# Kernel optimization log

Hardware: AMD Instinct MI355X
Metric: run time of the kernel (lower is better)

The kernel has to match this reference:

```python
import jax, jax.numpy as jnp
import numpy as np

N = 4096          # batch of anchors
D = 128           # embedding dim
M = 4             # instances per class (balanced batch) -> 3 positives per anchor
MARGIN = 1.0
INF = jnp.float32(1e30)


def setup_inputs() -> dict:
    key = jax.random.key(0)
    inputs = jax.random.normal(key, (N, D), dtype=jnp.float32)
    targets = (jnp.arange(N, dtype=jnp.int32) // M).astype(jnp.int32)
    return {"inputs": inputs, "targets": targets}


def _forward(inputs, targets, key):
    n = inputs.shape[0]
    k_pos = M - 1            # positives per anchor (and multinomial draw count)
    k_neg = n - M            # negatives per anchor

    # euclidean_dist: ||xi||^2 + ||xj||^2 - 2 xi.xj, clamped and sqrt'ed
    sq = jnp.sum(inputs * inputs, axis=1)
    dist = sq[:, None] + sq[None, :] - 2.0 * (inputs @ inputs.T)
    dist = jnp.sqrt(jnp.clip(dist, 1e-12, None))

    same = targets[:, None] == targets[None, :]
    eye = jnp.eye(n, dtype=bool)
    pos_mask = same & ~eye
    neg_mask = ~same

    # balanced batch -> exactly k_pos positives / k_neg negatives per row;
    # push non-members to +inf and sort (original sorts pos/neg pairs anyway)
    pos_sorted = jnp.sort(jnp.where(pos_mask, dist, INF), axis=1)[:, :k_pos]  # [n, 3]
    neg_sorted = jnp.sort(jnp.where(neg_mask, dist, INF), axis=1)[:, :k_neg]  # [n, n-M]

    pos3 = pos_sorted[:, :3]  # pos_pair[:3]

    # GaussDistribution over the (sorted) negative row
    neg_mean = jnp.mean(neg_sorted, axis=1, keepdims=True)
    neg_std = jnp.sqrt(jnp.mean((neg_sorted - neg_mean) ** 2, axis=1, keepdims=True))
    # prob = exp((x-mean)^2 / (2 std^2)); use log-weights for Gumbel-top-k
    log_prob = (neg_sorted - neg_mean) ** 2 / (2.0 * neg_std ** 2)

    # multinomial without replacement == top-k of log_prob + Gumbel noise
    g = jax.random.gumbel(key, neg_sorted.shape, dtype=jnp.float32)
    _, idx = jax.lax.top_k(log_prob + g, k_pos)                 # [n, 3]
    sampled = jnp.take_along_axis(neg_sorted, idx, axis=1)      # [n, 3]

    # masked_select(neg_pair < pos_pair[-1] + 0.05) -> boolean keep mask
    kept = sampled < (pos3[:, -1:] + 0.05)
    cnt = jnp.sum(kept, axis=1)
    any_kept = cnt > 0

    # pos_loss = 0.5*mean(log(1+exp(-2*(margin - pos))))
    pos_loss = 0.5 * jnp.mean(jax.nn.softplus(-2.0 * (MARGIN - pos3)), axis=1)
    # neg_loss = 0.05*mean over kept of log(1+exp(20*(margin - neg)))
    neg_terms = jax.nn.softplus(20.0 * (MARGIN - sampled))
    neg_loss = 0.05 * jnp.sum(jnp.where(kept, neg_terms, 0.0), axis=1) / jnp.maximum(cnt, 1)

    row_loss = jnp.where(any_kept, pos_loss + neg_loss, 0.0)
    loss = jnp.sum(row_loss) / n

    # err: pos_pair[0] < neg_pair[0] - 0.1 (first kept sampled negative)
    first_idx = jnp.argmax(kept, axis=1)
    neg0 = jnp.take_along_axis(sampled, first_idx[:, None], axis=1)[:, 0]
    err = jnp.sum((any_kept & (pos3[:, 0] < neg0 - 0.1)).astype(jnp.float32))
    prec = 1.0 - err / n

    pos_d = jnp.mean(pos_sorted)
    neg_d = jnp.mean(neg_sorted)
    return loss, prec, pos_d, neg_d


def reference(inputs, targets):
    key = jax.random.key(42)  # fixed sampling key (torch.multinomial analogue)
    return _forward(inputs, targets, key)
```

## Files before the change

kernel.cpp:

```cpp
#include <hip/hip_runtime.h>
#include <stdint.h>

#define NROW 4096
#define NDIM 128
#define KNEG 4092
#define INF_VAL 1e30f
#define BUCKETS 2048
#define PLO 384
#define PHI 3712
#define GTOT ((size_t)NROW * (size_t)KNEG)

typedef __attribute__((ext_vector_type(8))) short short8;
typedef __attribute__((ext_vector_type(4))) float f32x4;

__device__ __forceinline__ uint32_t rotl32(uint32_t v, int d) {
  return (v << d) | (v >> (32 - d));
}

__device__ __forceinline__ void threefry2x32(uint32_t x0, uint32_t x1,
                                             uint32_t& y0, uint32_t& y1) {
  const uint32_t k0 = 0u, k1 = 42u;
  const uint32_t k2 = 0x1BD11BDAu ^ k0 ^ k1;
  uint32_t v0 = x0 + k0, v1 = x1 + k1;
#define TF_R(r) v0 += v1; v1 = rotl32(v1, r); v1 ^= v0;
  TF_R(13) TF_R(15) TF_R(26) TF_R(6)
  v0 += k1; v1 += k2 + 1u;
  TF_R(17) TF_R(29) TF_R(16) TF_R(24)
  v0 += k2; v1 += k0 + 2u;
  TF_R(13) TF_R(15) TF_R(26) TF_R(6)
  v0 += k0; v1 += k1 + 3u;
  TF_R(17) TF_R(29) TF_R(16) TF_R(24)
  v0 += k1; v1 += k2 + 4u;
  TF_R(13) TF_R(15) TF_R(26) TF_R(6)
  v0 += k2; v1 += k0 + 5u;
#undef TF_R
  y0 = v0; y1 = v1;
}

__device__ __forceinline__ float gumbel_ref(uint32_t f) {
  uint32_t y0, y1;
  threefry2x32(0u, f, y0, y1);
  uint32_t m = y1 >> 9;
  float u;
  if (m == 0u) u = 1.17549435e-38f;
  else u = __uint_as_float(m | 0x3f800000u) - 1.0f;
  return -__logf(-__logf(u));
}

__device__ __forceinline__ float softplus_ref(float x) {
  return fmaxf(x, 0.0f) + log1pf(expf(-fabsf(x)));
}

__device__ __forceinline__ int bucket_lin(float x, float mean, float invw) {
  float b = (x - mean) * invw + 1024.0f;
  b = fminf(fmaxf(b, 0.0f), 2047.0f);
  return (int)b;
}

__global__ __launch_bounds__(64) void prep_kernel(const float* __restrict__ X,
                                                  float* __restrict__ sq,
                                                  ushort* __restrict__ Xbf) {
  int i = blockIdx.x;
  int lane = threadIdx.x;
  float2 v = ((const float2*)(X + (size_t)i * NDIM))[lane];
  float s = v.x * v.x + v.y * v.y;
  for (int o = 32; o > 0; o >>= 1) s += __shfl_down(s, o);
  if (lane == 0) sq[i] = s;
  uint32_t ux = __float_as_uint(v.x);
  uint32_t uy = __float_as_uint(v.y);
  ux += 0x7fffu + ((ux >> 16) & 1u);
  uy += 0x7fffu + ((uy >> 16) & 1u);
  ushort2 h;
  h.x = (ushort)(ux >> 16);
  h.y = (ushort)(uy >> 16);
  ((ushort2*)(Xbf + (size_t)i * NDIM))[lane] = h;
}

__global__ __launch_bounds__(256) void gumbel_kernel(float* __restrict__ g) {
  uint32_t b0 = (uint32_t)blockIdx.x * 4096u;
#pragma unroll
  for (int q = 0; q < 4; ++q) {
    uint32_t f0 = b0 + (uint32_t)q * 1024u + (uint32_t)threadIdx.x * 4u;
    float4 v;
    v.x = gumbel_ref(f0 + 0u);
    v.y = gumbel_ref(f0 + 1u);
    v.z = gumbel_ref(f0 + 2u);
    v.w = gumbel_ref(f0 + 3u);
    *(float4*)(g + f0) = v;
  }
}

#define DSTR 68
__global__ __launch_bounds__(256) void dist_mfma(const ushort* __restrict__ Xbf,
                                                 const float* __restrict__ sq,
                                                 float* __restrict__ dist) {
  __shared__ ushort Als[128 * DSTR];
  __shared__ ushort Bls[128 * DSTR];
  const int tid = threadIdx.x;
  const int wave = tid >> 6, lane = tid & 63;
  const int q = lane >> 4, ln = lane & 15;
  const int bi = blockIdx.y, bj = blockIdx.x;
  const ushort* Ag = Xbf + (size_t)bi * 128 * NDIM;
  const ushort* Bg = Xbf + (size_t)bj * 128 * NDIM;

  f32x4 acc[8][2];
#pragma unroll
  for (int mt = 0; mt < 8; ++mt)
#pragma unroll
    for (int nt = 0; nt < 2; ++nt) acc[mt][nt] = (f32x4){0.f, 0.f, 0.f, 0.f};

  for (int kh = 0; kh < 2; ++kh) {
    if (kh) __syncthreads();
#pragma unroll
    for (int t = 0; t < 4; ++t) {
      int c = tid + 256 * t;
      int r = c >> 3, k8 = (c & 7) << 3;
      *(short8*)&Als[r * DSTR + k8] =
          *(const short8*)(Ag + (size_t)r * NDIM + kh * 64 + k8);
      *(short8*)&Bls[r * DSTR + k8] =
          *(const short8*)(Bg + (size_t)r * NDIM + kh * 64 + k8);
    }
    __syncthreads();
#pragma unroll
    for (int k0 = 0; k0 < 64; k0 += 32) {
      int kf = k0 + q * 8;
      short8 a[8], b[2];
#pragma unroll
      for (int mt = 0; mt < 8; ++mt)
        a[mt] = *(const short8*)&Als[(mt * 16 + ln) * DSTR + kf];
#pragma unroll
      for (int nt = 0; nt < 2; ++nt)
        b[nt] = *(const short8*)&Bls[(wave * 32 + nt * 16 + ln) * DSTR + kf];
#pragma unroll
      for (int mt = 0; mt < 8; ++mt)
#pragma unroll
        for (int nt = 0; nt < 2; ++nt)
          acc[mt][nt] = __builtin_amdgcn_mfma_f32_16x16x32_bf16(
              a[mt], b[nt], acc[mt][nt], 0, 0, 0);
    }
  }

  float sqj[2];
#pragma unroll
  for (int nt = 0; nt < 2; ++nt)
    sqj[nt] = sq[bj * 128 + wave * 32 + nt * 16 + ln];
#pragma unroll
  for (int mt = 0; mt < 8; ++mt) {
    int ibase = bi * 128 + mt * 16 + q * 4;
#pragma unroll
    for (int r = 0; r < 4; ++r) {
      int i = ibase + r;
      float sqi = sq[i];
#pragma unroll
      for (int nt = 0; nt < 2; ++nt) {
        int j = bj * 128 + wave * 32 + nt * 16 + ln;
        float d = sqi + sqj[nt] - 2.0f * acc[mt][nt][r];
        dist[(size_t)i * NROW + j] = sqrtf(fmaxf(d, 1e-12f));
      }
    }
  }
}

__global__ __launch_bounds__(256) void row_kernel(const float* __restrict__ dist,
                                                  const float* __restrict__ G,
                                                  float4* __restrict__ part) {
  __shared__ alignas(16) float sorted[NROW];
  __shared__ alignas(16) int base[BUCKETS];
  __shared__ float wredf[8];
  __shared__ int wtot[4];
  __shared__ float s_pos[3];
  __shared__ float s_sel[3];

  float* cscore = (float*)base;
  float* cx     = (float*)base + 768;
  int*   crank  = (int*)sorted;
  float* redf   = sorted + 1024;
  int*   redi   = (int*)(sorted + 1280);
  int*   redi2  = (int*)(sorted + 1536);

  const int i = blockIdx.x;
  const int tid = threadIdx.x;
  const int lane = tid & 63, wid = tid >> 6;
  const float* row = dist + (size_t)i * NROW;
  const int gbase = i & ~3;

  float x[16];
  {
    const float4* r4 = (const float4*)row;
#pragma unroll
    for (int q4 = 0; q4 < 4; ++q4) {
      float4 f = r4[tid * 4 + q4];
      x[q4 * 4 + 0] = f.x; x[q4 * 4 + 1] = f.y;
      x[q4 * 4 + 2] = f.z; x[q4 * 4 + 3] = f.w;
    }
  }

  if (tid == (gbase >> 4)) {
    float p[3]; int np = 0;
#pragma unroll
    for (int qq = 0; qq < 4; ++qq) {
      int j = gbase + qq;
      if (j != i) p[np++] = x[j & 15];
    }
    float a = p[0], b = p[1], c = p[2], t_;
    if (a > b) { t_ = a; a = b; b = t_; }
    if (b > c) { t_ = b; b = c; c = t_; }
    if (a > b) { t_ = a; a = b; b = t_; }
    s_pos[0] = a; s_pos[1] = b; s_pos[2] = c;
  }

#pragma unroll
  for (int qq = 0; qq < 16; ++qq) {
    int j = tid * 16 + qq;
    if ((j >> 2) == (i >> 2)) x[qq] = INF_VAL;
  }

  float ls = 0.f;
#pragma unroll
  for (int qq = 0; qq < 16; ++qq) if (x[qq] < 1e29f) ls += x[qq];
  for (int o = 32; o > 0; o >>= 1) ls += __shfl_down(ls, o);
  if (lane == 0) wredf[wid] = ls;
  __syncthreads();
  const float negsum = wredf[0] + wredf[1] + wredf[2] + wredf[3];
  const float mean = negsum / (float)KNEG;

  float ls2 = 0.f;
#pragma unroll
  for (int qq = 0; qq < 16; ++qq)
    if (x[qq] < 1e29f) { float z = x[qq] - mean; ls2 += z * z; }
  for (int o = 32; o > 0; o >>= 1) ls2 += __shfl_down(ls2, o);
  if (lane == 0) wredf[4 + wid] = ls2;
  __syncthreads();
  const float var = (wredf[4] + wredf[5] + wredf[6] + wredf[7]) / (float)KNEG;
  const float stdv = sqrtf(var);
  const float rdenom = __frcp_rn(2.0f * stdv * stdv);
  const float invw = 256.0f / stdv;

  {
    int4* b4 = (int4*)base;
    b4[tid] = (int4){0, 0, 0, 0};
    b4[tid + 256] = (int4){0, 0, 0, 0};
  }
  __syncthreads();
  int bkt[16];
#pragma unroll
  for (int qq = 0; qq < 16; ++qq) {
    bkt[qq] = bucket_lin(x[qq], mean, invw);
    atomicAdd(&base[bkt[qq]], 1);
  }
  __syncthreads();

  int c8[8]; int lsum = 0;
#pragma unroll
  for (int qq = 0; qq < 8; ++qq) {
    int t_ = base[tid * 8 + qq];
    c8[qq] = lsum; lsum += t_;
  }
  int incl = lsum;
  for (int off = 1; off < 64; off <<= 1) {
    int o = __shfl_up(incl, off);
    if (lane >= off) incl += o;
  }
  if (lane == 63) wtot[wid] = incl;
  __syncthreads();
  int excl = incl - lsum;
#pragma unroll
  for (int w = 0; w < 4; ++w) if (w < wid) excl += wtot[w];
#pragma unroll
  for (int qq = 0; qq < 8; ++qq) base[tid * 8 + qq] = excl + c8[qq];
  __syncthreads();

#pragma unroll
  for (int qq = 0; qq < 16; ++qq) {
    int p = atomicAdd(&base[bkt[qq]], 1);
    sorted[p] = x[qq];
  }
  __syncthreads();

  const uint32_t fbase = (uint32_t)i * (uint32_t)KNEG;
  const float* grow = G ? (G + fbase) : nullptr;
  float t0s = -1e38f, t1s = -1e38f, t2s = -1e38f;
  int   t0r = 0x7fffffff, t1r = 0x7fffffff, t2r = 0x7fffffff;
  float t0x = 0.f, t1x = 0.f, t2x = 0.f;
#pragma unroll
  for (int qq = 0; qq < 16; ++qq) {
    int p = tid + 256 * qq;
    float xv = sorted[p];
    int rank = p;
    if ((qq <= 1 || qq >= 14) && (p < PLO || p >= PHI)) {
      int b = bucket_lin(xv, mean, invw);
      int s0 = (b == 0) ? 0 : base[b - 1];
      int e0 = base[b];
      int c = 0;
      for (int u = s0; u < e0; ++u) {
        float o = sorted[u];
        c += (o < xv || (o == xv && u < p)) ? 1 : 0;
      }
      rank = s0 + c;
    }
    if (rank < KNEG) {
      float z = xv - mean;
      float gv = grow ? grow[rank] : gumbel_ref(fbase + (uint32_t)rank);
      float sv = fmaf(z * z, rdenom, gv);
      if (sv > t2s || (sv == t2s && rank < t2r)) {
        t2s = sv; t2r = rank; t2x = xv;
        if (t2s > t1s || (t2s == t1s && t2r < t1r)) {
          float ts = t1s; int tr = t1r; float tx = t1x;
          t1s = t2s; t1r = t2r; t1x = t2x; t2s = ts; t2r = tr; t2x = tx;
        }
        if (t1s > t0s || (t1s == t0s && t1r < t0r)) {
          float ts = t0s; int tr = t0r; float tx = t0x;
          t0s = t1s; t0r = t1r; t0x = t1x; t1s = ts; t1r = tr; t1x = tx;
        }
      }
    }
  }
  __syncthreads();

  cscore[tid * 3 + 0] = t0s; crank[tid * 3 + 0] = t0r; cx[tid * 3 + 0] = t0x;
  cscore[tid * 3 + 1] = t1s; crank[tid * 3 + 1] = t1r; cx[tid * 3 + 1] = t1x;
  cscore[tid * 3 + 2] = t2s; crank[tid * 3 + 2] = t2r; cx[tid * 3 + 2] = t2x;
  __syncthreads();

  for (int t = 0; t < 3; ++t) {
    float bs = -1e38f; int br = 0x7fffffff; int bidx = 0;
    for (int k = tid; k < 768; k += 256) {
      float s_ = cscore[k]; int r_ = crank[k];
      if (s_ > bs || (s_ == bs && r_ < br)) { bs = s_; br = r_; bidx = k; }
    }
    redf[tid] = bs; redi[tid] = br; redi2[tid] = bidx;
    __syncthreads();
    if (tid < 64) {
      float s0_ = redf[tid]; int r0_ = redi[tid]; int i0_ = redi2[tid];
#pragma unroll
      for (int o = 64; o < 256; o += 64) {
        float s1 = redf[tid + o]; int r1 = redi[tid + o];
        if (s1 > s0_ || (s1 == s0_ && r1 < r0_)) {
          s0_ = s1; r0_ = r1; i0_ = redi2[tid + o];
        }
      }
      for (int off = 32; off > 0; off >>= 1) {
        float s1 = __shfl_down(s0_, off);
        int r1 = __shfl_down(r0_, off);
        int i1 = __shfl_down(i0_, off);
        if (s1 > s0_ || (s1 == s0_ && r1 < r0_)) { s0_ = s1; r0_ = r1; i0_ = i1; }
      }
      if (tid == 0) { s_sel[t] = cx[i0_]; cscore[i0_] = -1e38f; }
    }
    __syncthreads();
  }

  if (tid == 0) {
    float p0 = s_pos[0], p1 = s_pos[1], p2 = s_pos[2];
    float thr = p2 + 0.05f;
    float samp[3]; bool kept[3]; int cnt = 0;
#pragma unroll
    for (int t = 0; t < 3; ++t) {
      samp[t] = s_sel[t];
      kept[t] = samp[t] < thr;
      cnt += kept[t] ? 1 : 0;
    }
    bool any = cnt > 0;
    float pos_loss = 0.5f *
        (softplus_ref(-2.0f * (1.0f - p0)) + softplus_ref(-2.0f * (1.0f - p1)) +
         softplus_ref(-2.0f * (1.0f - p2))) / 3.0f;
    float nsum = 0.0f;
#pragma unroll
    for (int t = 0; t < 3; ++t)
      if (kept[t]) nsum += softplus_ref(20.0f * (1.0f - samp[t]));
    float neg_loss = 0.05f * nsum / (float)(cnt > 0 ? cnt : 1);
    float row_loss = any ? (pos_loss + neg_loss) : 0.0f;
    int first = kept[0] ? 0 : (kept[1] ? 1 : (kept[2] ? 2 : 0));
    float neg0 = samp[first];
    float errv = (any && (p0 < neg0 - 0.1f)) ? 1.0f : 0.0f;
    float4 pr;
    pr.x = row_loss; pr.y = errv; pr.z = p0 + p1 + p2; pr.w = negsum;
    part[i] = pr;
  }
}

__global__ __launch_bounds__(256) void reduce_kernel(const float4* __restrict__ part,
                                                     float* __restrict__ out) {
  __shared__ double wsum[4][4];
  const int tid = threadIdx.x;
  const int lane = tid & 63, wid = tid >> 6;
  double s0 = 0.0, s1 = 0.0, s2 = 0.0, s3 = 0.0;
  for (int k = tid; k < NROW; k += 256) {
    float4 v = part[k];
    s0 += (double)v.x; s1 += (double)v.y; s2 += (double)v.z; s3 += (double)v.w;
  }
  for (int o = 32; o > 0; o >>= 1) {
    s0 += __shfl_down(s0, o); s1 += __shfl_down(s1, o);
    s2 += __shfl_down(s2, o); s3 += __shfl_down(s3, o);
  }
  if (lane == 0) {
    wsum[wid][0] = s0; wsum[wid][1] = s1; wsum[wid][2] = s2; wsum[wid][3] = s3;
  }
  __syncthreads();
  if (tid == 0) {
    double a0 = wsum[0][0] + wsum[1][0] + wsum[2][0] + wsum[3][0];
    double a1 = wsum[0][1] + wsum[1][1] + wsum[2][1] + wsum[3][1];
    double a2 = wsum[0][2] + wsum[1][2] + wsum[2][2] + wsum[3][2];
    double a3 = wsum[0][3] + wsum[1][3] + wsum[2][3] + wsum[3][3];
    out[0] = (float)(a0 / (double)NROW);
    out[1] = (float)(1.0 - a1 / (double)NROW);
    out[2] = (float)(a2 / ((double)NROW * 3.0));
    out[3] = (float)(a3 / ((double)NROW * (double)KNEG));
  }
}

extern "C" void kernel_launch(void* const* d_in, const int* in_sizes, int n_in,
                              void* d_out, int out_size, void* d_ws, size_t ws_size,
                              hipStream_t stream) {
  (void)in_sizes; (void)n_in; (void)out_size;
  const float* X = (const float*)d_in[0];
  float* out = (float*)d_out;
  char* ws = (char*)d_ws;

  float* dist = (float*)ws;
  size_t off = (size_t)NROW * NROW * sizeof(float);
  float* sq = (float*)(ws + off);            off += NROW * sizeof(float);
  ushort* Xbf = (ushort*)(ws + off);         off += (size_t)NROW * NDIM * sizeof(ushort);
  float4* part = (float4*)(ws + off);        off += (size_t)NROW * sizeof(float4);
  float* G = nullptr;
  if (ws_size >= off + GTOT * sizeof(float)) G = (float*)(ws + off);

  prep_kernel<<<NROW, 64, 0, stream>>>(X, sq, Xbf);
  if (G) gumbel_kernel<<<KNEG, 256, 0, stream>>>(G);
  dim3 gb(NROW / 128, NROW / 128);
  dist_mfma<<<gb, 256, 0, stream>>>(Xbf, sq, dist);
  row_kernel<<<NROW, 256, 0, stream>>>(dist, G, part);
  reduce_kernel<<<1, 256, 0, stream>>>(part, out);
}
```

Before: 184.8 us.

## Fuse Gumbel generation into distance kernel and vectorize distance stores

Merges the separate Gumbel-noise kernel into the distance GEMM launch as extra blocks, so the compute-heavy RNG work can overlap with the MFMA distance tiles and one launch is removed. It also permutes the B-tile column mapping so each lane owns two adjacent columns, which turns scalar dist stores into float2 stores. In exchange, both workloads share one grid and its LDS allocation, which may reduce occupancy for the Gumbel blocks.

New measurement: 180.4 us. 1.02x faster.

```diff
diff --git a/kernel.cpp b/kernel.cpp
--- a/kernel.cpp
+++ b/kernel.cpp
@@ -9,6 +9,8 @@
 #define PLO 384
 #define PHI 3712
 #define GTOT ((size_t)NROW * (size_t)KNEG)
+#define DISTBLKS 1024
+#define GUMBLKS KNEG
 
 typedef __attribute__((ext_vector_type(8))) short short8;
 typedef __attribute__((ext_vector_type(4))) float f32x4;
@@ -76,30 +78,35 @@
   ((ushort2*)(Xbf + (size_t)i * NDIM))[lane] = h;
 }
 
-__global__ __launch_bounds__(256) void gumbel_kernel(float* __restrict__ g) {
-  uint32_t b0 = (uint32_t)blockIdx.x * 4096u;
-#pragma unroll
-  for (int q = 0; q < 4; ++q) {
-    uint32_t f0 = b0 + (uint32_t)q * 1024u + (uint32_t)threadIdx.x * 4u;
-    float4 v;
-    v.x = gumbel_ref(f0 + 0u);
-    v.y = gumbel_ref(f0 + 1u);
-    v.z = gumbel_ref(f0 + 2u);
-    v.w = gumbel_ref(f0 + 3u);
-    *(float4*)(g + f0) = v;
-  }
-}
-
 #define DSTR 68
-__global__ __launch_bounds__(256) void dist_mfma(const ushort* __restrict__ Xbf,
-                                                 const float* __restrict__ sq,
-                                                 float* __restrict__ dist) {
+__global__ __launch_bounds__(256) void dist_gumbel(const ushort* __restrict__ Xbf,
+                                                   const float* __restrict__ sq,
+                                                   float* __restrict__ dist,
+                                                   float* __restrict__ g) {
   __shared__ ushort Als[128 * DSTR];
   __shared__ ushort Bls[128 * DSTR];
   const int tid = threadIdx.x;
+
+  if (blockIdx.x >= DISTBLKS) {
+    if (g) {
+      uint32_t b0 = (uint32_t)(blockIdx.x - DISTBLKS) * 4096u;
+#pragma unroll
+      for (int q = 0; q < 4; ++q) {
+        uint32_t f0 = b0 + (uint32_t)q * 1024u + (uint32_t)tid * 4u;
+        float4 v;
+        v.x = gumbel_ref(f0 + 0u);
+        v.y = gumbel_ref(f0 + 1u);
+        v.z = gumbel_ref(f0 + 2u);
+        v.w = gumbel_ref(f0 + 3u);
+        *(float4*)(g + f0) = v;
+      }
+    }
+    return;
+  }
+
+  const int bi = blockIdx.x >> 5, bj = blockIdx.x & 31;
   const int wave = tid >> 6, lane = tid & 63;
   const int q = lane >> 4, ln = lane & 15;
-  const int bi = blockIdx.y, bj = blockIdx.x;
   const ushort* Ag = Xbf + (size_t)bi * 128 * NDIM;
   const ushort* Bg = Xbf + (size_t)bj * 128 * NDIM;
 
@@ -130,7 +137,7 @@
         a[mt] = *(const short8*)&Als[(mt * 16 + ln) * DSTR + kf];
 #pragma unroll
       for (int nt = 0; nt < 2; ++nt)
-        b[nt] = *(const short8*)&Bls[(wave * 32 + nt * 16 + ln) * DSTR + kf];
+        b[nt] = *(const short8*)&Bls[(wave * 32 + 2 * ln + nt) * DSTR + kf];
 #pragma unroll
       for (int mt = 0; mt < 8; ++mt)
 #pragma unroll
@@ -140,10 +147,8 @@
     }
   }
 
-  float sqj[2];
-#pragma unroll
-  for (int nt = 0; nt < 2; ++nt)
-    sqj[nt] = sq[bj * 128 + wave * 32 + nt * 16 + ln];
+  const int jcol = bj * 128 + wave * 32 + 2 * ln;
+  float sqj0 = sq[jcol], sqj1 = sq[jcol + 1];
 #pragma unroll
   for (int mt = 0; mt < 8; ++mt) {
     int ibase = bi * 128 + mt * 16 + q * 4;
@@ -151,12 +156,10 @@
     for (int r = 0; r < 4; ++r) {
       int i = ibase + r;
       float sqi = sq[i];
-#pragma unroll
-      for (int nt = 0; nt < 2; ++nt) {
-        int j = bj * 128 + wave * 32 + nt * 16 + ln;
-        float d = sqi + sqj[nt] - 2.0f * acc[mt][nt][r];
-        dist[(size_t)i * NROW + j] = sqrtf(fmaxf(d, 1e-12f));
-      }
+      float2 o;
+      o.x = sqrtf(fmaxf(sqi + sqj0 - 2.0f * acc[mt][0][r], 1e-12f));
+      o.y = sqrtf(fmaxf(sqi + sqj1 - 2.0f * acc[mt][1][r], 1e-12f));
+      *(float2*)(dist + (size_t)i * NROW + jcol) = o;
     }
   }
 }
@@ -426,9 +429,7 @@
   if (ws_size >= off + GTOT * sizeof(float)) G = (float*)(ws + off);
 
   prep_kernel<<<NROW, 64, 0, stream>>>(X, sq, Xbf);
-  if (G) gumbel_kernel<<<KNEG, 256, 0, stream>>>(G);
-  dim3 gb(NROW / 128, NROW / 128);
-  dist_mfma<<<gb, 256, 0, stream>>>(Xbf, sq, dist);
+  dist_gumbel<<<DISTBLKS + (G ? GUMBLKS : 0), 256, 0, stream>>>(Xbf, sq, dist, G);
   row_kernel<<<NROW, 256, 0, stream>>>(dist, G, part);
   reduce_kernel<<<1, 256, 0, stream>>>(part, out);
 }
```
